# Performance work log

Measured on AMD Instinct MI355X. Metric: run time of the kernel, lower is better.

## Reference

```python
import jax, jax.numpy as jnp
import numpy as np

N, K = 50000, 10      # nodes, sampled neighbors (num_sample)
V, F = 200000, 128    # embedding table rows, input_dim
H = 64                # hidden per direction (hidden_dim=128, bidirectional)


def setup_inputs() -> dict:
    key = jax.random.key(0)
    ks = jax.random.split(key, 12)
    s = 1.0 / np.sqrt(H)  # torch LSTM init: U(-1/sqrt(H), 1/sqrt(H))
    u = lambda k, shape: jax.random.uniform(k, shape, jnp.float32, -s, s)
    return {
        "neigh_idx": jax.random.randint(ks[0], (N, K), 0, V),
        "embed_table": jax.random.normal(ks[1], (V, F), jnp.float32) * 0.02,
        # forward-direction LSTM params (torch gate order: i, f, g, o)
        "Wih_f": u(ks[2], (4 * H, F)), "Whh_f": u(ks[3], (4 * H, H)),
        "bih_f": u(ks[4], (4 * H,)),   "bhh_f": u(ks[5], (4 * H,)),
        # backward-direction LSTM params
        "Wih_b": u(ks[6], (4 * H, F)), "Whh_b": u(ks[7], (4 * H, H)),
        "bih_b": u(ks[8], (4 * H,)),   "bhh_b": u(ks[9], (4 * H,)),
    }


def _lstm_scan(x, Wih, Whh, bih, bhh):
    """x: [N,K,F] -> hidden outputs [N,K,H] (single direction)."""
    n = x.shape[0]
    # precompute input projections for all steps: [N,K,4H]
    xg = jnp.einsum('nkf,gf->nkg', x, Wih) + bih + bhh
    h0 = jnp.zeros((n, H), x.dtype)
    c0 = jnp.zeros((n, H), x.dtype)

    def step(carry, xt):
        h, c = carry
        gates = xt + h @ Whh.T
        i, f, g, o = jnp.split(gates, 4, axis=-1)
        i = jax.nn.sigmoid(i)
        f = jax.nn.sigmoid(f)
        g = jnp.tanh(g)
        o = jax.nn.sigmoid(o)
        c = f * c + i * g
        h = o * jnp.tanh(c)
        return (h, c), h

    _, hs = jax.lax.scan(step, (h0, c0), jnp.swapaxes(xg, 0, 1))  # [K,N,H]
    return jnp.swapaxes(hs, 0, 1)


def reference(neigh_idx, embed_table, Wih_f, Whh_f, bih_f, bhh_f,
              Wih_b, Whh_b, bih_b, bhh_b):
    x = embed_table[neigh_idx]  # gather: [N,K,F]
    # forward direction: last-step hidden
    h_f = _lstm_scan(x, Wih_f, Whh_f, bih_f, bhh_f)[:, -1, :]
    # backward direction processes reversed sequence; torch output[:, -1] of the
    # backward stream is its hidden after processing only element K-1 (step 0).
    h_b = _lstm_scan(x[:, ::-1, :], Wih_b, Whh_b, bih_b, bhh_b)[:, 0, :]
    return jnp.concatenate([h_f, h_b], axis=-1)  # [N, 2H]
```

## Files before the change

kernel.cpp:

```cpp
#include <hip/hip_runtime.h>
#include <hip/hip_bf16.h>


#define NN 50000
#define KK 10
#define FF 128
#define HH 64

#define WS_WIH_F 0
#define WS_WHH_F 32768
#define WS_WIH_B 49152

#define NPB 32
#define NT 1563
#define GRID 521
#define HS 72

typedef __bf16 bf16x8 __attribute__((ext_vector_type(8)));
typedef float f32x4 __attribute__((ext_vector_type(4)));
typedef float f32x2 __attribute__((ext_vector_type(2)));

#if __has_builtin(__builtin_amdgcn_exp2f)
#define EXP2(x) __builtin_amdgcn_exp2f(x)
#else
#define EXP2(x) exp2f(x)
#endif

__device__ __forceinline__ float fast_sig(float x) {
    float e = EXP2(x * -1.44269504f);
    return __builtin_amdgcn_rcpf(1.0f + e);
}
__device__ __forceinline__ float fast_tanh(float x) {
    float e = EXP2(x * 2.88539008f);
    return 1.0f - 2.0f * __builtin_amdgcn_rcpf(e + 1.0f);
}
__device__ __forceinline__ f32x2 sig2(f32x2 x) {
    f32x2 t = x * -1.44269504f;
    f32x2 e = {EXP2(t.x), EXP2(t.y)};
    f32x2 d = e + 1.0f;
    return (f32x2){__builtin_amdgcn_rcpf(d.x), __builtin_amdgcn_rcpf(d.y)};
}
__device__ __forceinline__ f32x2 tanh2(f32x2 x) {
    f32x2 t = x * 2.88539008f;
    f32x2 e = {EXP2(t.x), EXP2(t.y)};
    f32x2 d = e + 1.0f;
    f32x2 r = {__builtin_amdgcn_rcpf(d.x), __builtin_amdgcn_rcpf(d.y)};
    return 1.0f - 2.0f * r;
}

__global__ void cvt_weights_kernel(const float* __restrict__ Wih_f,
                                   const float* __restrict__ Whh_f,
                                   const float* __restrict__ Wih_b,
                                   __bf16* __restrict__ ws) {
    int i = blockIdx.x * 256 + threadIdx.x;
    ws[WS_WIH_F + i] = (__bf16)Wih_f[i];
    if (i < 16384) ws[WS_WHH_F + i] = (__bf16)Whh_f[i];
    ws[WS_WIH_B + i] = (__bf16)Wih_b[i];
}

__global__ __launch_bounds__(256, 2) void lstm_agg_kernel(
    const int* __restrict__ nidx,
    const float* __restrict__ tab,
    const float* __restrict__ bih_f,
    const float* __restrict__ bhh_f,
    const float* __restrict__ bih_b,
    const float* __restrict__ bhh_b,
    const __bf16* __restrict__ ws,
    float* __restrict__ out)
{
    __shared__ __bf16 x_lds[2][NPB * FF];
    __shared__ __bf16 h_lds[2][NPB * HS];
    __shared__ int    gq[NPB][KK];

    const int tid  = threadIdx.x;
    const int w    = tid >> 6;
    const int lane = tid & 63;
    const int q    = lane >> 4;
    const int c    = lane & 15;
    const int koff = q * 8;
    const int sw = (c & 7) << 4;

    const int srow  = tid >> 3;
    const int spart = tid & 7;
    const int swW   = (srow & 7) << 4;

    f32x4 G[4];
    auto stage_load = [&](int kidx) {
        const float* src = tab + (size_t)gq[srow][kidx] * FF + spart * 16;
#pragma unroll
        for (int j = 0; j < 4; ++j) G[j] = *(const f32x4*)(src + j * 4);
    };
    auto stage_write = [&](int b) {
        bf16x8 v0, v1;
#pragma unroll
        for (int e = 0; e < 4; ++e) {
            v0[e]     = (__bf16)G[0][e];
            v0[4 + e] = (__bf16)G[1][e];
            v1[e]     = (__bf16)G[2][e];
            v1[4 + e] = (__bf16)G[3][e];
        }
        char* row = (char*)(x_lds[b] + srow * FF);
        *(bf16x8*)(row + ((spart * 32)      ^ swW)) = v0;
        *(bf16x8*)(row + ((spart * 32 + 16) ^ swW)) = v1;
    };

    bf16x8 bWih[4][4], bWhh[4][2];
#pragma unroll
    for (int g = 0; g < 4; ++g) {
        int row = (g * 4 + w) * 16 + c;
#pragma unroll
        for (int kk = 0; kk < 4; ++kk)
            bWih[g][kk] = *(const bf16x8*)(ws + WS_WIH_F + row * FF + kk * 32 + koff);
#pragma unroll
        for (int kk = 0; kk < 2; ++kk)
            bWhh[g][kk] = *(const bf16x8*)(ws + WS_WHH_F + row * HH + kk * 32 + koff);
    }
    float bias[4];
#pragma unroll
    for (int g = 0; g < 4; ++g) {
        int u = g * 64 + w * 16 + c;
        bias[g] = bih_f[u] + bhh_f[u];
    }

    for (int tile = blockIdx.x; tile < NT; tile += GRID) {
        const int node_base = tile * NPB;

        __syncthreads();
        for (int i = tid; i < NPB * KK; i += 256) {
            int r = i / KK, k = i - r * KK;
            int node = min(node_base + r, NN - 1);
            gq[r][k] = nidx[node * KK + k];
        }
        __syncthreads();

        stage_load(0);
        __builtin_amdgcn_sched_barrier(0);
        stage_write(0);
        __syncthreads();

        f32x4 acc[4][2];
        float cst[2][4];
#pragma unroll
        for (int r = 0; r < 2; ++r)
#pragma unroll
            for (int e = 0; e < 4; ++e) cst[r][e] = 0.0f;

#pragma unroll 2
        for (int k = 0; k < KK; ++k) {
            const int cur = k & 1;
            if (k + 1 < KK) {
                stage_load(k + 1);
                __builtin_amdgcn_sched_barrier(0);
            }

#pragma unroll
            for (int g = 0; g < 4; ++g)
#pragma unroll
                for (int r = 0; r < 2; ++r)
                    acc[g][r] = (f32x4){bias[g], bias[g], bias[g], bias[g]};

            __builtin_amdgcn_s_setprio(1);
            const char* xb = (const char*)x_lds[cur];
#pragma unroll
            for (int r = 0; r < 2; ++r) {
                const char* rp = xb + (r * 16 + c) * 256;
                bf16x8 xa[4];
#pragma unroll
                for (int kk = 0; kk < 4; ++kk)
                    xa[kk] = *(const bf16x8*)(rp + ((kk * 64 + q * 16) ^ sw));
#pragma unroll
                for (int g = 0; g < 4; ++g)
#pragma unroll
                    for (int kk = 0; kk < 4; ++kk)
                        acc[g][r] = __builtin_amdgcn_mfma_f32_16x16x32_bf16(
                            xa[kk], bWih[g][kk], acc[g][r], 0, 0, 0);
            }
            if (k > 0) {
                const __bf16* hb = h_lds[(k - 1) & 1];
#pragma unroll
                for (int r = 0; r < 2; ++r) {
                    bf16x8 ha[2];
#pragma unroll
                    for (int kk = 0; kk < 2; ++kk)
                        ha[kk] = *(const bf16x8*)(hb + (r * 16 + c) * HS + kk * 32 + koff);
#pragma unroll
                    for (int g = 0; g < 4; ++g)
#pragma unroll
                        for (int kk = 0; kk < 2; ++kk)
                            acc[g][r] = __builtin_amdgcn_mfma_f32_16x16x32_bf16(
                                ha[kk], bWhh[g][kk], acc[g][r], 0, 0, 0);
                }
            }
            __builtin_amdgcn_s_setprio(0);

            const bool last = (k == KK - 1);
            __bf16* hw = h_lds[k & 1];
#pragma unroll
            for (int r = 0; r < 2; ++r)
#pragma unroll
                for (int p = 0; p < 2; ++p) {
                    f32x2 ai = {acc[0][r][2 * p], acc[0][r][2 * p + 1]};
                    f32x2 af = {acc[1][r][2 * p], acc[1][r][2 * p + 1]};
                    f32x2 ag = {acc[2][r][2 * p], acc[2][r][2 * p + 1]};
                    f32x2 ao = {acc[3][r][2 * p], acc[3][r][2 * p + 1]};
                    f32x2 gi = sig2(ai);
                    f32x2 gf = sig2(af);
                    f32x2 gg = tanh2(ag);
                    f32x2 go = sig2(ao);
                    f32x2 cc = {cst[r][2 * p], cst[r][2 * p + 1]};
                    f32x2 cn = gf * cc + gi * gg;
                    cst[r][2 * p]     = cn.x;
                    cst[r][2 * p + 1] = cn.y;
                    f32x2 h = go * tanh2(cn);
                    hw[(r * 16 + q * 4 + 2 * p)     * HS + w * 16 + c] = (__bf16)h.x;
                    hw[(r * 16 + q * 4 + 2 * p + 1) * HS + w * 16 + c] = (__bf16)h.y;
                    if (last) {
                        int node = node_base + r * 16 + q * 4 + 2 * p;
                        if (node < NN)     out[(size_t)node * 128 + w * 16 + c] = h.x;
                        if (node + 1 < NN) out[(size_t)(node + 1) * 128 + w * 16 + c] = h.y;
                    }
                }

            if (k + 1 < KK) stage_write(cur ^ 1);
            __syncthreads();
        }

        {
            const int gb[3] = {0, 2, 3};
            const char* xb = (const char*)x_lds[(KK - 1) & 1];
            f32x4 ab[3][2];
#pragma unroll
            for (int j = 0; j < 3; ++j) {
                int row = (gb[j] * 4 + w) * 16 + c;
                bf16x8 bW[4];
#pragma unroll
                for (int kk = 0; kk < 4; ++kk)
                    bW[kk] = *(const bf16x8*)(ws + WS_WIH_B + row * FF + kk * 32 + koff);
                int u = gb[j] * 64 + w * 16 + c;
                float bb = bih_b[u] + bhh_b[u];
#pragma unroll
                for (int r = 0; r < 2; ++r) {
                    f32x4 a = (f32x4){bb, bb, bb, bb};
                    const char* rp = xb + (r * 16 + c) * 256;
#pragma unroll
                    for (int kk = 0; kk < 4; ++kk) {
                        bf16x8 xa = *(const bf16x8*)(rp + ((kk * 64 + q * 16) ^ sw));
                        a = __builtin_amdgcn_mfma_f32_16x16x32_bf16(xa, bW[kk], a, 0, 0, 0);
                    }
                    ab[j][r] = a;
                }
            }
#pragma unroll
            for (int r = 0; r < 2; ++r)
#pragma unroll
                for (int reg = 0; reg < 4; ++reg) {
                    float gi = fast_sig(ab[0][r][reg]);
                    float gg = fast_tanh(ab[1][r][reg]);
                    float go = fast_sig(ab[2][r][reg]);
                    float hb2 = go * fast_tanh(gi * gg);
                    int node = node_base + r * 16 + q * 4 + reg;
                    if (node < NN) out[(size_t)node * 128 + 64 + w * 16 + c] = hb2;
                }
        }
    }
}

extern "C" void kernel_launch(void* const* d_in, const int* in_sizes, int n_in,
                              void* d_out, int out_size, void* d_ws, size_t ws_size,
                              hipStream_t stream) {
    const int*   nidx  = (const int*)d_in[0];
    const float* tab   = (const float*)d_in[1];
    const float* Wih_f = (const float*)d_in[2];
    const float* Whh_f = (const float*)d_in[3];
    const float* bih_f = (const float*)d_in[4];
    const float* bhh_f = (const float*)d_in[5];
    const float* Wih_b = (const float*)d_in[6];
    const float* bih_b = (const float*)d_in[8];
    const float* bhh_b = (const float*)d_in[9];
    __bf16* ws  = (__bf16*)d_ws;
    float*  out = (float*)d_out;

    hipLaunchKernelGGL(cvt_weights_kernel, dim3(32768 / 256), dim3(256), 0, stream,
                       Wih_f, Whh_f, Wih_b, ws);

    hipLaunchKernelGGL(lstm_agg_kernel, dim3(GRID), dim3(256), 0, stream,
                       nidx, tab, bih_f, bhh_f, bih_b, bhh_b, ws, out);
}
```

Baseline: 261.3 us.

## Deepen gather prefetch to two steps with dual register buffers and lighter barriers

Embedding-row gathers are now issued two LSTM steps ahead using two alternating register buffers (GA/GB), so global load latency overlaps two steps of MFMA/activation work instead of one. __syncthreads is replaced by an explicit lgkmcnt wait plus s_barrier, which avoids waiting on outstanding global (vmcnt) loads at each step barrier. The grid is also changed from 521 to 512 blocks. The extra 16 floats of live registers raise pressure under launch_bounds(256,2) and may cause spills.

Result: faster. 228.6 us (-12.5%).

```diff
diff --git a/kernel.cpp b/kernel.cpp
--- a/kernel.cpp
+++ b/kernel.cpp
@@ -13,7 +13,7 @@
 
 #define NPB 32
 #define NT 1563
-#define GRID 521
+#define GRID 512
 #define HS 72
 
 typedef __bf16 bf16x8 __attribute__((ext_vector_type(8)));
@@ -57,6 +57,35 @@
     if (i < 16384) ws[WS_WHH_F + i] = (__bf16)Whh_f[i];
     ws[WS_WIH_B + i] = (__bf16)Wih_b[i];
 }
+
+#define STAGE_LOAD(Gs, kidx)                                                  \
+    do {                                                                      \
+        const float* _src = tab + (size_t)gq[srow][(kidx)] * FF + spart * 16; \
+        _Pragma("unroll")                                                     \
+        for (int _j = 0; _j < 4; ++_j) Gs[_j] = *(const f32x4*)(_src + _j * 4);\
+    } while (0)
+
+#define STAGE_WRITE(Gs, b)                                                    \
+    do {                                                                      \
+        bf16x8 _v0, _v1;                                                      \
+        _Pragma("unroll")                                                     \
+        for (int _e = 0; _e < 4; ++_e) {                                      \
+            _v0[_e]     = (__bf16)Gs[0][_e];                                  \
+            _v0[4 + _e] = (__bf16)Gs[1][_e];                                  \
+            _v1[_e]     = (__bf16)Gs[2][_e];                                  \
+            _v1[4 + _e] = (__bf16)Gs[3][_e];                                  \
+        }                                                                     \
+        char* _row = (char*)(x_lds[(b)] + srow * FF);                         \
+        *(bf16x8*)(_row + ((spart * 32)      ^ swW)) = _v0;                   \
+        *(bf16x8*)(_row + ((spart * 32 + 16) ^ swW)) = _v1;                   \
+    } while (0)
+
+#define STEP_BARRIER()                                                        \
+    do {                                                                      \
+        asm volatile("s_waitcnt lgkmcnt(0)" ::: "memory");                    \
+        __builtin_amdgcn_s_barrier();                                         \
+        __builtin_amdgcn_sched_barrier(0);                                    \
+    } while (0)
 
 __global__ __launch_bounds__(256, 2) void lstm_agg_kernel(
     const int* __restrict__ nidx,
@@ -84,25 +113,7 @@
     const int spart = tid & 7;
     const int swW   = (srow & 7) << 4;
 
-    f32x4 G[4];
-    auto stage_load = [&](int kidx) {
-        const float* src = tab + (size_t)gq[srow][kidx] * FF + spart * 16;
-#pragma unroll
-        for (int j = 0; j < 4; ++j) G[j] = *(const f32x4*)(src + j * 4);
-    };
-    auto stage_write = [&](int b) {
-        bf16x8 v0, v1;
-#pragma unroll
-        for (int e = 0; e < 4; ++e) {
-            v0[e]     = (__bf16)G[0][e];
-            v0[4 + e] = (__bf16)G[1][e];
-            v1[e]     = (__bf16)G[2][e];
-            v1[4 + e] = (__bf16)G[3][e];
-        }
-        char* row = (char*)(x_lds[b] + srow * FF);
-        *(bf16x8*)(row + ((spart * 32)      ^ swW)) = v0;
-        *(bf16x8*)(row + ((spart * 32 + 16) ^ swW)) = v1;
-    };
+    f32x4 GA[4], GB[4];
 
     bf16x8 bWih[4][4], bWhh[4][2];
 #pragma unroll
@@ -133,10 +144,11 @@
         }
         __syncthreads();
 
-        stage_load(0);
+        STAGE_LOAD(GA, 0);
+        STAGE_LOAD(GB, 1);
         __builtin_amdgcn_sched_barrier(0);
-        stage_write(0);
-        __syncthreads();
+        STAGE_WRITE(GA, 0);
+        STEP_BARRIER();
 
         f32x4 acc[4][2];
         float cst[2][4];
@@ -148,8 +160,9 @@
 #pragma unroll 2
         for (int k = 0; k < KK; ++k) {
             const int cur = k & 1;
-            if (k + 1 < KK) {
-                stage_load(k + 1);
+            if (k + 2 < KK) {
+                if ((k & 1) == 0) STAGE_LOAD(GA, k + 2);
+                else              STAGE_LOAD(GB, k + 2);
                 __builtin_amdgcn_sched_barrier(0);
             }
 
@@ -221,8 +234,11 @@
                     }
                 }
 
-            if (k + 1 < KK) stage_write(cur ^ 1);
-            __syncthreads();
+            if (k + 1 < KK) {
+                if (((k + 1) & 1) == 0) STAGE_WRITE(GA, 0);
+                else                    STAGE_WRITE(GB, 1);
+            }
+            STEP_BARRIER();
         }
 
         {
```
